# Optimization experiments

Hardware: AMD Instinct MI355X
Metric: run time of the kernel (lower is better)

The kernel has to match this reference:

```python
import jax, jax.numpy as jnp
import numpy as np

N = 50000     # nodes
E = 800000    # edges (before self-loops)
DIN = 128     # input feature dim
DH = 16       # per-head hidden dim (layer 1)
H = 8         # heads (layer 1)
DOUT = 64     # output classes (layer 2, heads=1)


def setup_inputs() -> dict:
    key = jax.random.key(0)
    ks = jax.random.split(key, 10)
    def rn(k, shape, scale=0.1):
        return jax.random.normal(k, shape, dtype=jnp.float32) * scale
    x = jax.random.normal(ks[0], (N, DIN), dtype=jnp.float32)
    edge_index = jax.random.randint(ks[1], (2, E), 0, N, dtype=jnp.int64)
    return {
        "x": x,
        "edge_index": edge_index,
        "W1": rn(ks[2], (DIN, H * DH)),
        "a_src1": rn(ks[3], (H, DH)),
        "a_dst1": rn(ks[4], (H, DH)),
        "b1": jnp.zeros((H * DH,), jnp.float32),
        "W2": rn(ks[5], (H * DH, DOUT)),
        "a_src2": rn(ks[6], (1, DOUT)),
        "a_dst2": rn(ks[7], (1, DOUT)),
        "b2": jnp.zeros((DOUT,), jnp.float32),
    }


def gat_conv(x, src, dst, W, a_src, a_dst, b, heads, out_dim):
    """PyG-style GATConv: edge attention + segment softmax over dst + scatter-add."""
    n = x.shape[0]
    h = (x @ W).reshape(n, heads, out_dim)                 # [N, H, D]
    alpha_src = jnp.sum(h * a_src, axis=-1)                # [N, H]
    alpha_dst = jnp.sum(h * a_dst, axis=-1)                # [N, H]
    e = jax.nn.leaky_relu(alpha_src[src] + alpha_dst[dst], 0.2)  # [Etot, H]
    # numerically-stable segment softmax grouped by destination node
    m = jax.ops.segment_max(e, dst, num_segments=n)        # [N, H]
    ex = jnp.exp(e - m[dst])
    s = jax.ops.segment_sum(ex, dst, num_segments=n)       # [N, H]
    alpha = ex / (s[dst] + 1e-16)                          # [Etot, H]
    msg = h[src] * alpha[..., None]                        # [Etot, H, D]
    out = jax.ops.segment_sum(msg, dst, num_segments=n)    # [N, H, D]
    return out.reshape(n, heads * out_dim) + b


def reference(x, W1, a_src1, a_dst1, b1, W2, a_src2, a_dst2, b2, edge_index):
    # eval mode: F.dropout(p=0.6, training=False) is identity
    loop = jnp.arange(N, dtype=edge_index.dtype)
    src = jnp.concatenate([edge_index[0], loop])  # add_self_loops=True (PyG default)
    dst = jnp.concatenate([edge_index[1], loop])
    h = gat_conv(x, src, dst, W1, a_src1, a_dst1, b1, H, DH)
    h = jax.nn.elu(h)
    h = gat_conv(h, src, dst, W2, a_src2, a_dst2, b2, 1, DOUT)
    return (h, jax.nn.log_softmax(h, axis=1))
```

## Files before the change

kernel.cpp:

```cpp
#include <hip/hip_runtime.h>

#define NN 50000
#define EE 800000
#define ET (EE + NN)
#define NCH ((NN + 255) / 256)

typedef unsigned short ushort_t;

__device__ __forceinline__ float bf2f(ushort_t u) {
    return __uint_as_float(((unsigned int)u) << 16);
}
__device__ __forceinline__ ushort_t f2bf(float f) {
    unsigned int u = __float_as_uint(f);
    u += 0x7fffu + ((u >> 16) & 1u);
    return (ushort_t)(u >> 16);
}
__device__ __forceinline__ float lrelu(float e) {
    return fmaxf(e, 0.f) + 0.2f * fminf(e, 0.f);
}
__device__ __forceinline__ float ldf(const void* p, int i, bool f32) {
    return f32 ? ((const float*)p)[i] : bf2f(((const ushort_t*)p)[i]);
}

__global__ __launch_bounds__(256) void sniff_kernel(const unsigned int* xw, const int* eiw, int* flags) {
    __shared__ int cnt0, cnt1;
    int t = threadIdx.x;
    if (t == 0) { cnt0 = 0; cnt1 = 0; }
    __syncthreads();
    float v = __uint_as_float(xw[t]);
    float a = fabsf(v);
    if ((a > 1e-6f && a < 1e6f) || v == 0.f) atomicAdd(&cnt0, 1);
    if (eiw[2 * t + 1] != 0) atomicAdd(&cnt1, 1);
    __syncthreads();
    if (t == 0) {
        flags[0] = (cnt0 >= 192) ? 1 : 0;
        flags[1] = (cnt1 <= 16) ? 1 : 0;
    }
}

__device__ __forceinline__ void edge_sd(const int* ei, int i, bool i64, int& s, int& d) {
    if (i < EE) {
        if (i64) { s = ei[2 * i]; d = ei[2 * (EE + i)]; }
        else     { s = ei[i];     d = ei[EE + i]; }
    } else {
        s = d = i - EE;
    }
}

__global__ __launch_bounds__(256) void degree_rank_kernel(const int* ei, int* deg8, int* rank, const int* flags) {
    int i = blockIdx.x * 256 + threadIdx.x;
    if (i >= ET) return;
    bool i64 = flags[1] != 0;
    int g = blockIdx.x & 7;
    int s, d;
    edge_sd(ei, i, i64, s, d);
    rank[i] = atomicAdd(&deg8[(size_t)g * NN + d], 1);
}

__global__ __launch_bounds__(256) void scanA_kernel(const int* __restrict__ deg8, int* __restrict__ chunksum) {
    __shared__ int wsum[4];
    int t = threadIdx.x;
    int node = blockIdx.x * 256 + t;
    int v = 0;
    if (node < NN) {
        #pragma unroll
        for (int g = 0; g < 8; ++g) v += deg8[(size_t)g * NN + node];
    }
    int lane = t & 63, wid = t >> 6;
    #pragma unroll
    for (int off = 1; off < 64; off <<= 1) v += __shfl_xor(v, off);
    if (lane == 0) wsum[wid] = v;
    __syncthreads();
    if (t == 0) chunksum[blockIdx.x] = wsum[0] + wsum[1] + wsum[2] + wsum[3];
}

__global__ __launch_bounds__(256) void scanB_kernel(const int* __restrict__ chunksum, int* __restrict__ chunkoff,
                                                    int* __restrict__ rowptr) {
    __shared__ int wsum[4];
    int t = threadIdx.x;
    int lane = t & 63, wid = t >> 6;
    int v = (t < NCH) ? chunksum[t] : 0;
    int x = v;
    #pragma unroll
    for (int off = 1; off < 64; off <<= 1) {
        int y = __shfl_up(x, off);
        if (lane >= off) x += y;
    }
    if (lane == 63) wsum[wid] = x;
    __syncthreads();
    if (t < 4) {
        int s = wsum[t];
        #pragma unroll
        for (int off = 1; off < 4; off <<= 1) {
            int y = __shfl_up(s, off);
            if (t >= off) s += y;
        }
        wsum[t] = s;
    }
    __syncthreads();
    int incl = x + ((wid > 0) ? wsum[wid - 1] : 0);
    if (t < NCH) chunkoff[t] = incl - v;
    if (t == 255) rowptr[NN] = wsum[3];
}

__global__ __launch_bounds__(256) void scanC_kernel(int* __restrict__ deg8, int* __restrict__ rowptr,
                                                    const int* __restrict__ chunkoff) {
    __shared__ int wsum[4];
    int t = threadIdx.x;
    int node = blockIdx.x * 256 + t;
    int dv[8];
    int v = 0;
    if (node < NN) {
        #pragma unroll
        for (int g = 0; g < 8; ++g) {
            dv[g] = deg8[(size_t)g * NN + node];
            v += dv[g];
        }
    }
    int lane = t & 63, wid = t >> 6;
    int x = v;
    #pragma unroll
    for (int off = 1; off < 64; off <<= 1) {
        int y = __shfl_up(x, off);
        if (lane >= off) x += y;
    }
    if (lane == 63) wsum[wid] = x;
    __syncthreads();
    if (t < 4) {
        int s = wsum[t];
        #pragma unroll
        for (int off = 1; off < 4; off <<= 1) {
            int y = __shfl_up(s, off);
            if (t >= off) s += y;
        }
        wsum[t] = s;
    }
    __syncthreads();
    int excl = x - v + ((wid > 0) ? wsum[wid - 1] : 0);
    if (node < NN) {
        int run = chunkoff[blockIdx.x] + excl;
        rowptr[node] = run;
        #pragma unroll
        for (int g = 0; g < 8; ++g) {
            deg8[(size_t)g * NN + node] = run;
            run += dv[g];
        }
    }
}

__global__ __launch_bounds__(256) void fill_kernel(const int* ei, const int* deg8off, const int* rank,
                                                   int* col, const int* flags) {
    int i = blockIdx.x * 256 + threadIdx.x;
    if (i >= ET) return;
    bool i64 = flags[1] != 0;
    int g = blockIdx.x & 7;
    int s, d;
    edge_sd(ei, i, i64, s, d);
    col[deg8off[(size_t)g * NN + d] + rank[i]] = s;
}

#define FMA4(accv, wv, xs)                   \
    accv.x = fmaf(wv.x, xs, accv.x);         \
    accv.y = fmaf(wv.y, xs, accv.y);         \
    accv.z = fmaf(wv.z, xs, accv.z);         \
    accv.w = fmaf(wv.w, xs, accv.w);

template <bool AEXT, int NH>
__global__ __launch_bounds__(256) void gemm64_kernel(const void* Av, const void* Wv,
                                                     const void* a_src, const void* a_dst,
                                                     ushort_t* outb, float* asrc, float* adst,
                                                     int n, int wstride, int ostride,
                                                     const int* flags) {
    __shared__ __align__(16) float Wf[128 * 64];
    __shared__ __align__(16) float xT[128 * 64];
    bool f32 = flags[0] != 0;
    int t = threadIdx.x;
    int coloff = blockIdx.y * 64;

    if (f32) {
        const float* W = (const float*)Wv;
        for (int i = t; i < 2048; i += 256) {
            int k = i >> 4;
            int cp = i & 15;
            float4 wv = *(const float4*)(W + k * wstride + coloff + cp * 4);
            *(float4*)(&Wf[k * 64 + cp * 4]) = wv;
        }
    } else {
        const ushort_t* W = (const ushort_t*)Wv;
        for (int i = t; i < 4096; i += 256) {
            int k = i >> 5;
            int cp = i & 31;
            unsigned int v = *(const unsigned int*)(W + k * wstride + coloff + cp * 2);
            float2 w2 = make_float2(__uint_as_float(v << 16), __uint_as_float(v & 0xffff0000u));
            *(float2*)(&Wf[k * 64 + cp * 2]) = w2;
        }
    }

    int base = blockIdx.x * 64;
    int r = t & 63;
    int kc = t >> 6;
    int row = base + r;
    if (AEXT && !f32) {
        if (row < n) {
            const uint4* p = (const uint4*)((const ushort_t*)Av + (size_t)row * 128 + kc * 32);
            #pragma unroll
            for (int j = 0; j < 4; ++j) {
                uint4 q = p[j];
                int kb = kc * 32 + j * 8;
                xT[(kb + 0) * 64 + r] = __uint_as_float(q.x << 16);
                xT[(kb + 1) * 64 + r] = __uint_as_float(q.x & 0xffff0000u);
                xT[(kb + 2) * 64 + r] = __uint_as_float(q.y << 16);
                xT[(kb + 3) * 64 + r] = __uint_as_float(q.y & 0xffff0000u);
                xT[(kb + 4) * 64 + r] = __uint_as_float(q.z << 16);
                xT[(kb + 5) * 64 + r] = __uint_as_float(q.z & 0xffff0000u);
                xT[(kb + 6) * 64 + r] = __uint_as_float(q.w << 16);
                xT[(kb + 7) * 64 + r] = __uint_as_float(q.w & 0xffff0000u);
            }
        } else {
            #pragma unroll
            for (int j = 0; j < 32; ++j) xT[(kc * 32 + j) * 64 + r] = 0.f;
        }
    } else {
        if (row < n) {
            const float4* p = (const float4*)((const float*)Av + (size_t)row * 128 + kc * 32);
            #pragma unroll
            for (int j = 0; j < 8; ++j) {
                float4 q = p[j];
                int kb = kc * 32 + j * 4;
                xT[(kb + 0) * 64 + r] = q.x;
                xT[(kb + 1) * 64 + r] = q.y;
                xT[(kb + 2) * 64 + r] = q.z;
                xT[(kb + 3) * 64 + r] = q.w;
            }
        } else {
            #pragma unroll
            for (int j = 0; j < 32; ++j) xT[(kc * 32 + j) * 64 + r] = 0.f;
        }
    }
    __syncthreads();

    int cg = t & 15, rg = t >> 4;
    const float4* W4 = (const float4*)Wf;
    const float4* X4 = (const float4*)xT;
    float4 a0 = make_float4(0, 0, 0, 0), a1 = a0, a2 = a0, a3 = a0;
    #pragma unroll 4
    for (int k = 0; k < 128; ++k) {
        float4 wv = W4[k * 16 + cg];
        float4 xv = X4[k * 16 + rg];
        FMA4(a0, wv, xv.x)
        FMA4(a1, wv, xv.y)
        FMA4(a2, wv, xv.z)
        FMA4(a3, wv, xv.w)
    }

    int orow = base + rg * 4;
    int c0 = coloff + cg * 4;
    float4 av[4] = {a0, a1, a2, a3};
    #pragma unroll
    for (int j = 0; j < 4; ++j) {
        if (orow + j < n) {
            ushort4 o4;
            o4.x = f2bf(av[j].x); o4.y = f2bf(av[j].y);
            o4.z = f2bf(av[j].z); o4.w = f2bf(av[j].w);
            *(ushort4*)(outb + (size_t)(orow + j) * ostride + c0) = o4;
        }
    }

    float4 avs, avd;
    avs.x = ldf(a_src, c0 + 0, f32); avs.y = ldf(a_src, c0 + 1, f32);
    avs.z = ldf(a_src, c0 + 2, f32); avs.w = ldf(a_src, c0 + 3, f32);
    avd.x = ldf(a_dst, c0 + 0, f32); avd.y = ldf(a_dst, c0 + 1, f32);
    avd.z = ldf(a_dst, c0 + 2, f32); avd.w = ldf(a_dst, c0 + 3, f32);
    float ps[4], pd[4];
    #pragma unroll
    for (int j = 0; j < 4; ++j) {
        ps[j] = av[j].x * avs.x + av[j].y * avs.y + av[j].z * avs.z + av[j].w * avs.w;
        pd[j] = av[j].x * avd.x + av[j].y * avd.y + av[j].z * avd.z + av[j].w * avd.w;
    }
    const int span = (NH == 8) ? 4 : 16;
    #pragma unroll
    for (int stp = 1; stp < span; stp <<= 1) {
        #pragma unroll
        for (int j = 0; j < 4; ++j) {
            ps[j] += __shfl_xor(ps[j], stp);
            pd[j] += __shfl_xor(pd[j], stp);
        }
    }
    if ((cg & (span - 1)) == 0) {
        int hh = (NH == 8) ? (coloff / 16 + (cg >> 2)) : 0;
        #pragma unroll
        for (int j = 0; j < 4; ++j) {
            int rw = orow + j;
            if (rw < n) {
                asrc[(size_t)rw * NH + hh] = ps[j];
                adst[(size_t)rw * NH + hh] = pd[j];
            }
        }
    }
}

__global__ __launch_bounds__(256) void agg1_kernel(const int* __restrict__ rowptr, const int* __restrict__ col,
                                                   const ushort_t* __restrict__ h1b,
                                                   const float* __restrict__ asrc, const float* __restrict__ adst,
                                                   const void* b1, float* __restrict__ hmid, const int* flags) {
    __shared__ float wle[4][8 * 72];
    __shared__ int loff[4][64];
    bool f32 = flags[0] != 0;
    int lane = threadIdx.x & 63, wid = threadIdx.x >> 6;
    int d = blockIdx.x * 4 + wid;
    if (d >= NN) return;
    int start = rowptr[d], end = rowptr[d + 1];
    int hB = lane >> 3;
    const float4* dp = (const float4*)(adst + (size_t)d * 8);
    float4 ad0 = dp[0], ad1 = dp[1];
    const char* hb = (const char*)h1b + lane * 4;
    float acc0 = 0.f, acc1 = 0.f, ssum = 0.f;
    for (int chunk = start; chunk < end; chunk += 64) {
        int cnt = min(64, end - chunk);
        int c = (chunk + lane < end) ? col[chunk + lane] : 0;
        loff[wid][lane] = c << 8;
        if (lane < cnt) {
            const float4* ap = (const float4*)(asrc + (size_t)c * 8);
            float4 s0 = ap[0], s1 = ap[1];
            wle[wid][0 * 72 + lane] = __expf(lrelu(s0.x + ad0.x));
            wle[wid][1 * 72 + lane] = __expf(lrelu(s0.y + ad0.y));
            wle[wid][2 * 72 + lane] = __expf(lrelu(s0.z + ad0.z));
            wle[wid][3 * 72 + lane] = __expf(lrelu(s0.w + ad0.w));
            wle[wid][4 * 72 + lane] = __expf(lrelu(s1.x + ad1.x));
            wle[wid][5 * 72 + lane] = __expf(lrelu(s1.y + ad1.y));
            wle[wid][6 * 72 + lane] = __expf(lrelu(s1.z + ad1.z));
            wle[wid][7 * 72 + lane] = __expf(lrelu(s1.w + ad1.w));
        }
        #pragma unroll 4
        for (int j = 0; j < cnt; ++j) {
            int off = loff[wid][j];
            float ex = wle[wid][hB * 72 + j];
            unsigned int hv = *(const unsigned int*)(hb + off);
            ssum += ex;
            acc0 = fmaf(ex, __uint_as_float(hv << 16), acc0);
            acc1 = fmaf(ex, __uint_as_float(hv & 0xffff0000u), acc1);
        }
    }
    float inv = 1.f / (ssum + 1e-16f);
    float o0 = fmaf(acc0, inv, ldf(b1, lane * 2, f32));
    float o1 = fmaf(acc1, inv, ldf(b1, lane * 2 + 1, f32));
    o0 = (o0 > 0.f) ? o0 : (__expf(o0) - 1.f);
    o1 = (o1 > 0.f) ? o1 : (__expf(o1) - 1.f);
    *(float2*)(hmid + (size_t)d * 128 + lane * 2) = make_float2(o0, o1);
}

__global__ __launch_bounds__(256) void agg2_kernel(const int* __restrict__ rowptr, const int* __restrict__ col,
                                                   const ushort_t* __restrict__ h2b,
                                                   const float* __restrict__ asrc, const float* __restrict__ adst,
                                                   const void* b2, float* __restrict__ out, const int* flags) {
    __shared__ float wle[4][64];
    __shared__ int loff[4][64];
    bool f32 = flags[0] != 0;
    int lane = threadIdx.x & 63, wid = threadIdx.x >> 6;
    int d = blockIdx.x * 4 + wid;
    if (d >= NN) return;
    int start = rowptr[d], end = rowptr[d + 1];
    float ad = adst[d];
    const char* hb = (const char*)h2b + lane * 2;
    float acc = 0.f, ssum = 0.f;
    for (int chunk = start; chunk < end; chunk += 64) {
        int cnt = min(64, end - chunk);
        int c = (chunk + lane < end) ? col[chunk + lane] : 0;
        loff[wid][lane] = c << 7;
        if (lane < cnt) wle[wid][lane] = __expf(lrelu(asrc[c] + ad));
        #pragma unroll 4
        for (int j = 0; j < cnt; ++j) {
            int off = loff[wid][j];
            float ex = wle[wid][j];
            float hv = bf2f(*(const ushort_t*)(hb + off));
            ssum += ex;
            acc = fmaf(ex, hv, acc);
        }
    }
    float o = acc / (ssum + 1e-16f) + ldf(b2, lane, f32);
    float mm = o;
    #pragma unroll
    for (int off = 1; off < 64; off <<= 1) mm = fmaxf(mm, __shfl_xor(mm, off));
    float texp = __expf(o - mm);
    float ts = texp;
    #pragma unroll
    for (int off = 1; off < 64; off <<= 1) ts += __shfl_xor(ts, off);
    float ls = o - mm - __logf(ts);
    out[(size_t)d * 64 + lane] = o;
    out[(size_t)NN * 64 + (size_t)d * 64 + lane] = ls;
}

extern "C" void kernel_launch(void* const* d_in, const int* in_sizes, int n_in,
                              void* d_out, int out_size, void* d_ws, size_t ws_size,
                              hipStream_t stream) {
    const void* x   = d_in[0];
    const int*  ei  = (const int*)d_in[1];
    const void* W1  = d_in[2];
    const void* as1 = d_in[3];
    const void* ad1 = d_in[4];
    const void* b1  = d_in[5];
    const void* W2  = d_in[6];
    const void* as2 = d_in[7];
    const void* ad2 = d_in[8];
    const void* b2  = d_in[9];
    float* out = (float*)d_out;

    char* w = (char*)d_ws;
    auto alloc = [&](size_t bytes) {
        void* p = (void*)w;
        w += (bytes + 255) & ~(size_t)255;
        return p;
    };
    int* flags    = (int*)alloc(256);
    int* deg8     = (int*)alloc((size_t)8 * NN * 4);
    int* rowptr   = (int*)alloc((size_t)(NN + 1) * 4);
    int* chunksum = (int*)alloc((size_t)NCH * 4);
    int* chunkoff = (int*)alloc((size_t)NCH * 4);
    int* rank     = (int*)alloc((size_t)ET * 4);
    int* colx     = (int*)alloc((size_t)ET * 4);
    ushort_t* h1b = (ushort_t*)alloc((size_t)NN * 128 * 2);
    float* asrc1  = (float*)alloc((size_t)NN * 8 * 4);
    float* adst1  = (float*)alloc((size_t)NN * 8 * 4);
    float* hmid   = (float*)alloc((size_t)NN * 128 * 4);
    ushort_t* h2b = (ushort_t*)alloc((size_t)NN * 64 * 2);
    float* asrc2  = (float*)alloc((size_t)NN * 4);
    float* adst2  = (float*)alloc((size_t)NN * 4);

    sniff_kernel<<<1, 256, 0, stream>>>((const unsigned int*)x, ei, flags);

    hipMemsetAsync(deg8, 0, (size_t)8 * NN * 4, stream);
    degree_rank_kernel<<<(ET + 255) / 256, 256, 0, stream>>>(ei, deg8, rank, flags);
    scanA_kernel<<<NCH, 256, 0, stream>>>(deg8, chunksum);
    scanB_kernel<<<1, 256, 0, stream>>>(chunksum, chunkoff, rowptr);
    scanC_kernel<<<NCH, 256, 0, stream>>>(deg8, rowptr, chunkoff);
    fill_kernel<<<(ET + 255) / 256, 256, 0, stream>>>(ei, deg8, rank, colx, flags);

    dim3 g1((NN + 63) / 64, 2);
    gemm64_kernel<true, 8><<<g1, 256, 0, stream>>>(x, W1, as1, ad1, h1b, asrc1, adst1, NN, 128, 128, flags);
    agg1_kernel<<<(NN + 3) / 4, 256, 0, stream>>>(rowptr, colx, h1b, asrc1, adst1, b1, hmid, flags);

    dim3 g2((NN + 63) / 64, 1);
    gemm64_kernel<false, 1><<<g2, 256, 0, stream>>>((const void*)hmid, W2, as2, ad2, h2b, asrc2, adst2, NN, 64, 64, flags);
    agg2_kernel<<<(NN + 3) / 4, 256, 0, stream>>>(rowptr, colx, h2b, asrc2, adst2, b2, out, flags);
}
```

Baseline: 274.9 us.

## Replace FP32 FMA GEMMs with bf16 MFMA 16x16x32 matrix-core kernel

Replaces the shared-memory scalar-FMA GEMM used for both GAT projections with a kernel that uses the bf16 MFMA 16x16x32 instruction. W is staged transposed in LDS as bf16, and A rows are loaded directly into registers, converting from fp32 to bf16 when the input is float. Each block covers all output columns, so the layer-1 grid loses its column split, and the attention dot products are reduced with shuffles over the MFMA output layout. This is meant to cut the FP32 ALU and LDS cost of the GEMMs. In exchange, the input activations are rounded to bf16, which lowers accuracy, and the per-element output stores are no longer vectorized.

Result: no change. 271.5 us (-1.2%).

```diff
diff --git a/kernel.cpp b/kernel.cpp
--- a/kernel.cpp
+++ b/kernel.cpp
@@ -6,6 +6,8 @@
 #define NCH ((NN + 255) / 256)
 
 typedef unsigned short ushort_t;
+using bf16x8 = __attribute__((ext_vector_type(8))) short;
+using f32x4  = __attribute__((ext_vector_type(4))) float;
 
 __device__ __forceinline__ float bf2f(ushort_t u) {
     return __uint_as_float(((unsigned int)u) << 16);
@@ -159,141 +161,118 @@
     col[deg8off[(size_t)g * NN + d] + rank[i]] = s;
 }
 
-#define FMA4(accv, wv, xs)                   \
-    accv.x = fmaf(wv.x, xs, accv.x);         \
-    accv.y = fmaf(wv.y, xs, accv.y);         \
-    accv.z = fmaf(wv.z, xs, accv.z);         \
-    accv.w = fmaf(wv.w, xs, accv.w);
-
-template <bool AEXT, int NH>
-__global__ __launch_bounds__(256) void gemm64_kernel(const void* Av, const void* Wv,
-                                                     const void* a_src, const void* a_dst,
-                                                     ushort_t* outb, float* asrc, float* adst,
-                                                     int n, int wstride, int ostride,
-                                                     const int* flags) {
-    __shared__ __align__(16) float Wf[128 * 64];
-    __shared__ __align__(16) float xT[128 * 64];
+template <bool AEXT, int NCOL, int NH>
+__global__ __launch_bounds__(256) void mgemm_kernel(const void* Av, const void* Wv,
+                                                    const void* a_src, const void* a_dst,
+                                                    ushort_t* outb, float* asrc, float* adst,
+                                                    int n, const int* flags) {
+    constexpr int K = 128;
+    constexpr int NCT = NCOL / 16;
+    constexpr int WPAD = 136;
+    __shared__ __align__(16) ushort_t Wb[NCOL * WPAD];
     bool f32 = flags[0] != 0;
     int t = threadIdx.x;
-    int coloff = blockIdx.y * 64;
-
-    if (f32) {
-        const float* W = (const float*)Wv;
-        for (int i = t; i < 2048; i += 256) {
-            int k = i >> 4;
-            int cp = i & 15;
-            float4 wv = *(const float4*)(W + k * wstride + coloff + cp * 4);
-            *(float4*)(&Wf[k * 64 + cp * 4]) = wv;
+
+    for (int i = t; i < K * NCOL; i += 256) {
+        int k = i / NCOL, nc = i % NCOL;
+        Wb[nc * WPAD + k] = f32 ? f2bf(((const float*)Wv)[k * NCOL + nc])
+                                : ((const ushort_t*)Wv)[k * NCOL + nc];
+    }
+    __syncthreads();
+
+    int lane = t & 63, wid = t >> 6;
+    int m = lane & 15, quad = lane >> 4;
+    int rbase = blockIdx.x * 64 + wid * 16;
+    int row = rbase + m;
+    bool rok = row < n;
+
+    f32x4 acc[NCT];
+    #pragma unroll
+    for (int c = 0; c < NCT; ++c) acc[c] = (f32x4){0.f, 0.f, 0.f, 0.f};
+
+    #pragma unroll
+    for (int kk = 0; kk < K; kk += 32) {
+        bf16x8 af;
+        if (rok) {
+            if (AEXT && !f32) {
+                af = *(const bf16x8*)((const ushort_t*)Av + (size_t)row * K + kk + quad * 8);
+            } else {
+                const float* ap = (const float*)Av + (size_t)row * K + kk + quad * 8;
+                #pragma unroll
+                for (int j = 0; j < 8; ++j) af[j] = (short)f2bf(ap[j]);
+            }
+        } else {
+            af = (bf16x8){0, 0, 0, 0, 0, 0, 0, 0};
+        }
+        #pragma unroll
+        for (int c = 0; c < NCT; ++c) {
+            bf16x8 bf = *(const bf16x8*)(&Wb[(c * 16 + m) * WPAD + kk + quad * 8]);
+            acc[c] = __builtin_amdgcn_mfma_f32_16x16x32_bf16(af, bf, acc[c], 0, 0, 0);
+        }
+    }
+
+    int orow0 = rbase + quad * 4;
+    #pragma unroll
+    for (int c = 0; c < NCT; ++c) {
+        #pragma unroll
+        for (int r = 0; r < 4; ++r) {
+            int orow = orow0 + r;
+            if (orow < n) outb[(size_t)orow * NCOL + c * 16 + m] = f2bf(acc[c][r]);
+        }
+    }
+
+    if (NH == 8) {
+        #pragma unroll
+        for (int c = 0; c < NCT; ++c) {
+            float as = ldf(a_src, c * 16 + m, f32);
+            float ad = ldf(a_dst, c * 16 + m, f32);
+            float ps[4], pd[4];
+            #pragma unroll
+            for (int r = 0; r < 4; ++r) { ps[r] = acc[c][r] * as; pd[r] = acc[c][r] * ad; }
+            #pragma unroll
+            for (int stp = 1; stp < 16; stp <<= 1) {
+                #pragma unroll
+                for (int r = 0; r < 4; ++r) {
+                    ps[r] += __shfl_xor(ps[r], stp);
+                    pd[r] += __shfl_xor(pd[r], stp);
+                }
+            }
+            if (m == 0) {
+                #pragma unroll
+                for (int r = 0; r < 4; ++r) {
+                    int orow = orow0 + r;
+                    if (orow < n) {
+                        asrc[(size_t)orow * 8 + c] = ps[r];
+                        adst[(size_t)orow * 8 + c] = pd[r];
+                    }
+                }
+            }
         }
     } else {
-        const ushort_t* W = (const ushort_t*)Wv;
-        for (int i = t; i < 4096; i += 256) {
-            int k = i >> 5;
-            int cp = i & 31;
-            unsigned int v = *(const unsigned int*)(W + k * wstride + coloff + cp * 2);
-            float2 w2 = make_float2(__uint_as_float(v << 16), __uint_as_float(v & 0xffff0000u));
-            *(float2*)(&Wf[k * 64 + cp * 2]) = w2;
-        }
-    }
-
-    int base = blockIdx.x * 64;
-    int r = t & 63;
-    int kc = t >> 6;
-    int row = base + r;
-    if (AEXT && !f32) {
-        if (row < n) {
-            const uint4* p = (const uint4*)((const ushort_t*)Av + (size_t)row * 128 + kc * 32);
+        float ps[4] = {0.f, 0.f, 0.f, 0.f}, pd[4] = {0.f, 0.f, 0.f, 0.f};
+        #pragma unroll
+        for (int c = 0; c < NCT; ++c) {
+            float as = ldf(a_src, c * 16 + m, f32);
+            float ad = ldf(a_dst, c * 16 + m, f32);
             #pragma unroll
-            for (int j = 0; j < 4; ++j) {
-                uint4 q = p[j];
-                int kb = kc * 32 + j * 8;
-                xT[(kb + 0) * 64 + r] = __uint_as_float(q.x << 16);
-                xT[(kb + 1) * 64 + r] = __uint_as_float(q.x & 0xffff0000u);
-                xT[(kb + 2) * 64 + r] = __uint_as_float(q.y << 16);
-                xT[(kb + 3) * 64 + r] = __uint_as_float(q.y & 0xffff0000u);
-                xT[(kb + 4) * 64 + r] = __uint_as_float(q.z << 16);
-                xT[(kb + 5) * 64 + r] = __uint_as_float(q.z & 0xffff0000u);
-                xT[(kb + 6) * 64 + r] = __uint_as_float(q.w << 16);
-                xT[(kb + 7) * 64 + r] = __uint_as_float(q.w & 0xffff0000u);
-            }
-        } else {
+            for (int r = 0; r < 4; ++r) {
+                ps[r] = fmaf(acc[c][r], as, ps[r]);
+                pd[r] = fmaf(acc[c][r], ad, pd[r]);
+            }
+        }
+        #pragma unroll
+        for (int stp = 1; stp < 16; stp <<= 1) {
             #pragma unroll
-            for (int j = 0; j < 32; ++j) xT[(kc * 32 + j) * 64 + r] = 0.f;
-        }
-    } else {
-        if (row < n) {
-            const float4* p = (const float4*)((const float*)Av + (size_t)row * 128 + kc * 32);
+            for (int r = 0; r < 4; ++r) {
+                ps[r] += __shfl_xor(ps[r], stp);
+                pd[r] += __shfl_xor(pd[r], stp);
+            }
+        }
+        if (m == 0) {
             #pragma unroll
-            for (int j = 0; j < 8; ++j) {
-                float4 q = p[j];
-                int kb = kc * 32 + j * 4;
-                xT[(kb + 0) * 64 + r] = q.x;
-                xT[(kb + 1) * 64 + r] = q.y;
-                xT[(kb + 2) * 64 + r] = q.z;
-                xT[(kb + 3) * 64 + r] = q.w;
-            }
-        } else {
-            #pragma unroll
-            for (int j = 0; j < 32; ++j) xT[(kc * 32 + j) * 64 + r] = 0.f;
-        }
-    }
-    __syncthreads();
-
-    int cg = t & 15, rg = t >> 4;
-    const float4* W4 = (const float4*)Wf;
-    const float4* X4 = (const float4*)xT;
-    float4 a0 = make_float4(0, 0, 0, 0), a1 = a0, a2 = a0, a3 = a0;
-    #pragma unroll 4
-    for (int k = 0; k < 128; ++k) {
-        float4 wv = W4[k * 16 + cg];
-        float4 xv = X4[k * 16 + rg];
-        FMA4(a0, wv, xv.x)
-        FMA4(a1, wv, xv.y)
-        FMA4(a2, wv, xv.z)
-        FMA4(a3, wv, xv.w)
-    }
-
-    int orow = base + rg * 4;
-    int c0 = coloff + cg * 4;
-    float4 av[4] = {a0, a1, a2, a3};
-    #pragma unroll
-    for (int j = 0; j < 4; ++j) {
-        if (orow + j < n) {
-            ushort4 o4;
-            o4.x = f2bf(av[j].x); o4.y = f2bf(av[j].y);
-            o4.z = f2bf(av[j].z); o4.w = f2bf(av[j].w);
-            *(ushort4*)(outb + (size_t)(orow + j) * ostride + c0) = o4;
-        }
-    }
-
-    float4 avs, avd;
-    avs.x = ldf(a_src, c0 + 0, f32); avs.y = ldf(a_src, c0 + 1, f32);
-    avs.z = ldf(a_src, c0 + 2, f32); avs.w = ldf(a_src, c0 + 3, f32);
-    avd.x = ldf(a_dst, c0 + 0, f32); avd.y = ldf(a_dst, c0 + 1, f32);
-    avd.z = ldf(a_dst, c0 + 2, f32); avd.w = ldf(a_dst, c0 + 3, f32);
-    float ps[4], pd[4];
-    #pragma unroll
-    for (int j = 0; j < 4; ++j) {
-        ps[j] = av[j].x * avs.x + av[j].y * avs.y + av[j].z * avs.z + av[j].w * avs.w;
-        pd[j] = av[j].x * avd.x + av[j].y * avd.y + av[j].z * avd.z + av[j].w * avd.w;
-    }
-    const int span = (NH == 8) ? 4 : 16;
-    #pragma unroll
-    for (int stp = 1; stp < span; stp <<= 1) {
-        #pragma unroll
-        for (int j = 0; j < 4; ++j) {
-            ps[j] += __shfl_xor(ps[j], stp);
-            pd[j] += __shfl_xor(pd[j], stp);
-        }
-    }
-    if ((cg & (span - 1)) == 0) {
-        int hh = (NH == 8) ? (coloff / 16 + (cg >> 2)) : 0;
-        #pragma unroll
-        for (int j = 0; j < 4; ++j) {
-            int rw = orow + j;
-            if (rw < n) {
-                asrc[(size_t)rw * NH + hh] = ps[j];
-                adst[(size_t)rw * NH + hh] = pd[j];
+            for (int r = 0; r < 4; ++r) {
+                int orow = orow0 + r;
+                if (orow < n) { asrc[orow] = ps[r]; adst[orow] = pd[r]; }
             }
         }
     }
@@ -435,11 +414,10 @@
     scanC_kernel<<<NCH, 256, 0, stream>>>(deg8, rowptr, chunkoff);
     fill_kernel<<<(ET + 255) / 256, 256, 0, stream>>>(ei, deg8, rank, colx, flags);
 
-    dim3 g1((NN + 63) / 64, 2);
-    gemm64_kernel<true, 8><<<g1, 256, 0, stream>>>(x, W1, as1, ad1, h1b, asrc1, adst1, NN, 128, 128, flags);
+    int gblocks = (NN + 63) / 64;
+    mgemm_kernel<true, 128, 8><<<gblocks, 256, 0, stream>>>(x, W1, as1, ad1, h1b, asrc1, adst1, NN, flags);
     agg1_kernel<<<(NN + 3) / 4, 256, 0, stream>>>(rowptr, colx, h1b, asrc1, adst1, b1, hmid, flags);
 
-    dim3 g2((NN + 63) / 64, 1);
-    gemm64_kernel<false, 1><<<g2, 256, 0, stream>>>((const void*)hmid, W2, as2, ad2, h2b, asrc2, adst2, NN, 64, 64, flags);
+    mgemm_kernel<false, 64, 1><<<gblocks, 256, 0, stream>>>((const void*)hmid, W2, as2, ad2, h2b, asrc2, adst2, NN, flags);
     agg2_kernel<<<(NN + 3) / 4, 256, 0, stream>>>(rowptr, colx, h2b, asrc2, adst2, b2, out, flags);
 }
```
